# Kernel tuning notes

Hardware: AMD Instinct MI355X
Metric: run time of the kernel (lower is better)

## Reference

```python
import jax, jax.numpy as jnp
import numpy as np

MODES1 = 16
MODES2 = 16
KX_SIGMA = 1.0
B, T, H, W, C = 4, 32, 128, 128, 1

KY_KERNEL = np.array([[0.01, 0.02, 0.04, 0.02, 0.01],
                      [0.02, 0.06, 0.09, 0.06, 0.02],
                      [0.04, 0.09, 0.16, 0.09, 0.04],
                      [0.02, 0.06, 0.09, 0.06, 0.02],
                      [0.01, 0.02, 0.04, 0.02, 0.01]], dtype=np.float32)


def _spectral_mix(x, w1, w2):
    # x: (B,T,H,W,C); w1,w2: complex (C,C,m1,m2). FFT-mode-truncated mixing.
    b, t, h, w, c = x.shape
    xc = jnp.transpose(x, (0, 1, 4, 2, 3))            # (B,T,C,H,W)
    x_ft = jnp.fft.rfft2(xc)                          # (B,T,C,H,W//2+1)
    wr = w // 2 + 1
    out_ft = jnp.zeros((b, t, c, h, wr), dtype=x_ft.dtype)
    top = jnp.einsum('btixy,ioxy->btoxy', x_ft[:, :, :, :MODES1, :MODES2], w1)
    bot = jnp.einsum('btixy,ioxy->btoxy', x_ft[:, :, :, h - MODES1:, :MODES2], w2)
    out_ft = out_ft.at[:, :, :, :MODES1, :MODES2].set(top)
    out_ft = out_ft.at[:, :, :, h - MODES1:, :MODES2].set(bot)
    out = jnp.fft.irfft2(out_ft, s=(h, w))            # (B,T,C,H,W)
    return jnp.transpose(out, (0, 1, 3, 4, 2))


def _restricted_spectral(x, scalar):
    # diagonal (identity * scalar) spectral weights == scale truncated modes
    b, t, h, w, c = x.shape
    xc = jnp.transpose(x, (0, 1, 4, 2, 3))
    x_ft = jnp.fft.rfft2(xc)
    wr = w // 2 + 1
    out_ft = jnp.zeros((b, t, c, h, wr), dtype=x_ft.dtype)
    out_ft = out_ft.at[:, :, :, :MODES1, :MODES2].set(x_ft[:, :, :, :MODES1, :MODES2] * scalar)
    out_ft = out_ft.at[:, :, :, h - MODES1:, :MODES2].set(x_ft[:, :, :, h - MODES1:, :MODES2] * scalar)
    out = jnp.fft.irfft2(out_ft, s=(h, w))
    return jnp.transpose(out, (0, 1, 3, 4, 2))


def _circular_conv(value, kernel):
    # value: (B,T,H,W,1), kernel: (kh,kw); circular-pad cross-correlation
    b, t, h, w, _ = value.shape
    kh, kw = kernel.shape
    x = value.reshape(b * t, 1, h, w)
    xp = jnp.pad(x, ((0, 0), (0, 0), (kh // 2, kh - kh // 2 - 1), (kw // 2, kw - kw // 2 - 1)), mode='wrap')
    out = jax.lax.conv_general_dilated(xp, kernel[None, None], (1, 1), 'VALID',
                                       dimension_numbers=('NCHW', 'OIHW', 'NCHW'))
    return out.reshape(b, t, h, w, 1)


def setup_inputs() -> dict:
    key = jax.random.key(0)
    ks = jax.random.split(key, 10)
    z = jax.random.normal(ks[0], (B, T, 2 * H, W, C), dtype=jnp.float32)
    scale = 1.0 / (C * C)  # torch: scale * torch.rand(cfloat) -> uniform real & imag
    u = lambda k: scale * jax.random.uniform(k, (C, C, MODES1, MODES2), dtype=jnp.float32)
    return {
        'z': z,
        'qw1r': u(ks[1]), 'qw1i': u(ks[2]), 'qw2r': u(ks[3]), 'qw2i': u(ks[4]),
        'kw1r': u(ks[5]), 'kw1i': u(ks[6]), 'kw2r': u(ks[7]), 'kw2i': u(ks[8]),
        'icl_scalar': jnp.float32(0.1),
        'ky_kernel': jnp.asarray(KY_KERNEL),
    }


def reference(z, qw1r, qw1i, qw2r, qw2i, kw1r, kw1i, kw2r, kw2i, icl_scalar, ky_kernel):
    b, t, full_h, w, c = z.shape
    h = full_h // 2
    x, y = z[:, :, :h], z[:, :, h:]
    query = _spectral_mix(x, qw1r + 1j * qw1i, qw2r + 1j * qw2i)
    keyt = _spectral_mix(x, kw1r + 1j * kw1i, kw2r + 1j * kw2i)
    value = _restricted_spectral(y, icl_scalar)
    # laplacian kernel attention scores
    q_ = query.reshape(b, t, -1)
    k_ = keyt.reshape(b, t, -1)
    diff = q_[:, :, None, :] - k_[:, None, :, :]        # (B,T,T,H*W*C)
    l2 = jnp.sqrt(jnp.sum(diff * diff, axis=-1) + 1e-8)
    kx = jnp.exp(-l2 / KX_SIGMA)                         # (B,T,T)
    # mask: M @ kx zeros out last query row
    mask = jnp.concatenate([jnp.ones((t - 1,), jnp.float32), jnp.zeros((1,), jnp.float32)])
    kx = kx * mask[None, :, None]
    vc = _circular_conv(value, ky_kernel)                # (B,T,H,W,1)
    attn_y = jnp.einsum('bthwc,btq->bqhwc', vc, kx)      # (B,T,H,W,1)
    output = jnp.concatenate([jnp.zeros_like(x), attn_y], axis=2)
    return output, kx
```

## Files before the change

### kernel.cpp

```cpp
#include <hip/hip_runtime.h>
#include <math.h>

#define FVC_OFF   0
#define PHIQ_OFF  131072
#define PHIK_OFF  262144
#define OUT_KX_OFF 4194304

#define TWOPI_128 0.049087385212340517f

__global__ __launch_bounds__(256) void dft_rows_kernel(
    const float* __restrict__ z, float* __restrict__ Gout)
{
    __shared__ float ct[128], st[128];
    __shared__ float rows[16 * 132];
    __shared__ float2 tile[16 * 17];

    const int tid = threadIdx.x;
    const int img = blockIdx.x >> 3;
    const int c0  = blockIdx.x & 7;
    const int bt  = img & 127;
    const int isY = img >> 7;

    if (tid < 128) {
        float s, c;
        sincosf((float)tid * TWOPI_128, &s, &c);
        ct[tid] = c; st[tid] = s;
    }
    const float* xim = z + (size_t)bt * 32768 + (size_t)isY * 16384 + (size_t)c0 * 2048;
    {
        int q0 = tid, q1 = tid + 256;
        float4 a = *(const float4*)(xim + (q0 >> 5) * 128 + (q0 & 31) * 4);
        float4 b = *(const float4*)(xim + (q1 >> 5) * 128 + (q1 & 31) * 4);
        *(float4*)(rows + (q0 >> 5) * 132 + (q0 & 31) * 4) = a;
        *(float4*)(rows + (q1 >> 5) * 132 + (q1 & 31) * 4) = b;
    }
    __syncthreads();

    const int v  = tid & 15;
    const int hl = tid >> 4;
    float sr0 = 0.f, si0 = 0.f, sr1 = 0.f, si1 = 0.f;
    float sr2 = 0.f, si2 = 0.f, sr3 = 0.f, si3 = 0.f;
    const float4* rp = (const float4*)(rows + hl * 132);
    #pragma unroll 8
    for (int m = 0; m < 32; ++m) {
        float4 x4 = rp[m];
        int k = (v * m * 4) & 127;
        float c = ct[k], s = st[k];
        sr0 = fmaf(x4.x, c, sr0); si0 = fmaf(x4.x, s, si0);
        sr1 = fmaf(x4.y, c, sr1); si1 = fmaf(x4.y, s, si1);
        sr2 = fmaf(x4.z, c, sr2); si2 = fmaf(x4.z, s, si2);
        sr3 = fmaf(x4.w, c, sr3); si3 = fmaf(x4.w, s, si3);
    }
    float c1 = ct[v], s1 = st[v];
    float c2 = ct[(2 * v) & 127], s2 = st[(2 * v) & 127];
    float c3 = ct[(3 * v) & 127], s3 = st[(3 * v) & 127];
    float gr = sr0 + sr1 * c1 - si1 * s1 + sr2 * c2 - si2 * s2 + sr3 * c3 - si3 * s3;
    float gi = -(si0 + sr1 * s1 + si1 * c1 + sr2 * s2 + si2 * c2 + sr3 * s3 + si3 * c3);

    tile[v * 17 + hl] = make_float2(gr, gi);
    __syncthreads();
    const int vw = tid >> 4, hw = tid & 15;
    float2 val = tile[vw * 17 + hw];
    *(float2*)(Gout + (size_t)img * 4096 + vw * 256 + (c0 * 16 + hw) * 2) = val;
}

__global__ __launch_bounds__(128) void modes_kernel(
    const float* __restrict__ Gglob,
    const float* __restrict__ qw1r, const float* __restrict__ qw1i,
    const float* __restrict__ qw2r, const float* __restrict__ qw2i,
    const float* __restrict__ kw1r, const float* __restrict__ kw1i,
    const float* __restrict__ kw2r, const float* __restrict__ kw2i,
    const float* __restrict__ icl,  const float* __restrict__ ker,
    float* __restrict__ ws)
{
    __shared__ float ct[128], st[128];
    __shared__ float Gbuf[4 * 260];
    __shared__ float f0r[64], f0i[64];

    const int tid = threadIdx.x;
    const int img = blockIdx.x >> 2;
    const int vg  = blockIdx.x & 3;
    const int bt  = img & 127;
    const int isY = img >> 7;

    {
        float s, c;
        sincosf((float)tid * TWOPI_128, &s, &c);
        ct[tid] = c; st[tid] = s;
    }
    const float4* gsrc = (const float4*)(Gglob + (size_t)img * 4096 + (size_t)vg * 1024);
    {
        float4 a = gsrc[tid];
        float4 b = gsrc[tid + 128];
        *(float4*)(Gbuf + (tid >> 6) * 260 + (tid & 63) * 4) = a;
        *(float4*)(Gbuf + ((tid >> 6) + 2) * 260 + (tid & 63) * 4) = b;
    }
    __syncthreads();

    const int uu = tid & 31;
    const int vl = tid >> 5;
    const int v  = vg * 4 + vl;
    const int u  = (uu < 16) ? uu : uu + 96;

    float sr[4] = {0.f, 0.f, 0.f, 0.f}, si[4] = {0.f, 0.f, 0.f, 0.f};
    const float4* gp = (const float4*)(Gbuf + vl * 260);
    #pragma unroll 8
    for (int m = 0; m < 32; ++m) {
        float4 ga = gp[2 * m];
        float4 gb = gp[2 * m + 1];
        int k0 = (u * 4 * m) & 127;
        float c0 = ct[k0], s0 = st[k0];
        sr[0] = fmaf(ga.x, c0, fmaf(ga.y,  s0, sr[0]));
        si[0] = fmaf(ga.y, c0, fmaf(-ga.x, s0, si[0]));
        sr[1] = fmaf(ga.z, c0, fmaf(ga.w,  s0, sr[1]));
        si[1] = fmaf(ga.w, c0, fmaf(-ga.z, s0, si[1]));
        sr[2] = fmaf(gb.x, c0, fmaf(gb.y,  s0, sr[2]));
        si[2] = fmaf(gb.y, c0, fmaf(-gb.x, s0, si[2]));
        sr[3] = fmaf(gb.z, c0, fmaf(gb.w,  s0, sr[3]));
        si[3] = fmaf(gb.w, c0, fmaf(-gb.z, s0, si[3]));
    }
    float mr = sr[0], mi_ = si[0];
    #pragma unroll
    for (int j = 1; j < 4; ++j) {
        int k = (u * j) & 127;
        float cb = ct[k], sb = st[k];
        mr  += sr[j] * cb + si[j] * sb;
        mi_ += si[j] * cb - sr[j] * sb;
    }

    const int wi = (uu & 15) * 16 + v;

    if (!isY) {
        float a, bi_;
        if (uu < 16) { a = qw1r[wi]; bi_ = qw1i[wi]; }
        else         { a = qw2r[wi]; bi_ = qw2i[wi]; }
        float fqr = mr * a - mi_ * bi_;
        float fqi = mr * bi_ + mi_ * a;
        if (uu < 16) { a = kw1r[wi]; bi_ = kw1i[wi]; }
        else         { a = kw2r[wi]; bi_ = kw2i[wi]; }
        float fkr = mr * a - mi_ * bi_;
        float fki = mr * bi_ + mi_ * a;

        float* PQ = ws + PHIQ_OFF + (size_t)bt * 1024;
        float* PK = ws + PHIK_OFF + (size_t)bt * 1024;
        const float c2 = 0.011048543456039806f;
        if (v >= 1) {
            int o = ((v - 1) * 32 + uu) * 2;
            PQ[o] = c2 * fqr; PQ[o + 1] = c2 * fqi;
            PK[o] = c2 * fkr; PK[o + 1] = c2 * fki;
        } else {
            f0r[uu]      = fqr; f0i[uu]      = fqi;
            f0r[32 + uu] = fkr; f0i[32 + uu] = fki;
        }
        __syncthreads();
        if (vg == 0) {
            const float c1n = 0.0078125f;
            if (tid == 0) {
                PQ[960] = c1n * f0r[0];
                PK[960] = c1n * f0r[32];
            } else if (tid <= 15) {
                int uf = tid;
                float hr = 0.5f * (f0r[uf] + f0r[32 - uf]);
                float hi = 0.5f * (f0i[uf] - f0i[32 - uf]);
                int o = 961 + (uf - 1) * 2;
                PQ[o] = c2 * hr; PQ[o + 1] = c2 * hi;
                hr = 0.5f * (f0r[32 + uf] + f0r[32 + (32 - uf)]);
                hi = 0.5f * (f0i[32 + uf] - f0i[32 + (32 - uf)]);
                PK[o] = c2 * hr; PK[o + 1] = c2 * hi;
            } else if (tid == 16) {
                PQ[991] = c2 * 0.5f * f0r[16]; PQ[992] = -c2 * 0.5f * f0i[16];
                PK[991] = c2 * 0.5f * f0r[48]; PK[992] = -c2 * 0.5f * f0i[48];
            } else if (tid < 48) {
                PQ[993 + (tid - 17)] = 0.f;
                PK[993 + (tid - 17)] = 0.f;
            }
        }
    } else {
        float s = icl[0];
        float khr = 0.f, khi = 0.f;
        #pragma unroll
        for (int a2 = 0; a2 < 5; ++a2) {
            #pragma unroll
            for (int c3 = 0; c3 < 5; ++c3) {
                float kv = ker[a2 * 5 + c3];
                int e = (u * (a2 - 2) + v * (c3 - 2)) & 127;
                khr = fmaf(kv, ct[e], khr);
                khi = fmaf(kv, st[e], khi);
            }
        }
        const int slot = uu * 16 + v;
        float* FV = ws + FVC_OFF + (size_t)bt * 1024;
        FV[slot * 2]     = s * (mr * khr - mi_ * khi);
        FV[slot * 2 + 1] = s * (mr * khi + mi_ * khr);
    }
}

__global__ __launch_bounds__(256) void dist_mix_inv_kernel(
    const float* __restrict__ ws, float* __restrict__ out)
{
    __shared__ float ct[128], st[128];
    __shared__ float kxs[32];
    __shared__ float fmP[32 * 36];
    __shared__ float Ar[32 * 17], Ai[32 * 17];

    const int tid     = threadIdx.x;
    const int b       = blockIdx.x >> 7;
    const int rest    = blockIdx.x & 127;
    const int q       = rest >> 2;
    const int quarter = rest & 3;

    if (tid < 128) {
        float s, c;
        sincosf((float)tid * TWOPI_128, &s, &c);
        ct[tid] = c; st[tid] = s;
    }

    {
        const int t = tid >> 3, seg = tid & 7;
        const float4* qp = (const float4*)(ws + PHIQ_OFF + (size_t)(b * 32 + t) * 1024) + seg * 32;
        const float4* kp = (const float4*)(ws + PHIK_OFF + (size_t)(b * 32 + q) * 1024) + seg * 32;
        float acc = 0.f;
        #pragma unroll 8
        for (int d = 0; d < 32; ++d) {
            float4 qv = qp[d], kv = kp[d];
            float d0 = qv.x - kv.x, d1 = qv.y - kv.y;
            float d2 = qv.z - kv.z, d3 = qv.w - kv.w;
            acc = fmaf(d0, d0, acc); acc = fmaf(d1, d1, acc);
            acc = fmaf(d2, d2, acc); acc = fmaf(d3, d3, acc);
        }
        acc += __shfl_xor(acc, 1);
        acc += __shfl_xor(acc, 2);
        acc += __shfl_xor(acc, 4);
        if (seg == 0) {
            float l2  = sqrtf(acc + 1e-8f);
            float kxv = (t == 31) ? 0.f : expf(-l2);
            kxs[t] = kxv;
            if (quarter == 0)
                out[OUT_KX_OFF + (b * 32 + t) * 32 + q] = kxv;
        }
    }
    __syncthreads();

    {
        float4 acc = make_float4(0.f, 0.f, 0.f, 0.f);
        const float4* FV = (const float4*)(ws + FVC_OFF) + (size_t)b * 32 * 256;
        for (int i = 0; i < 31; ++i) {
            float kv = kxs[i];
            float4 f = FV[(size_t)i * 256 + tid];
            acc.x = fmaf(kv, f.x, acc.x);
            acc.y = fmaf(kv, f.y, acc.y);
            acc.z = fmaf(kv, f.z, acc.z);
            acc.w = fmaf(kv, f.w, acc.w);
        }
        int s0 = tid * 2;
        *(float4*)(fmP + (s0 >> 4) * 36 + (s0 & 15) * 2) = acc;
    }
    __syncthreads();

    {
        const int hl = tid >> 3;
        const int v0 = (tid & 7) * 2;
        const int h  = quarter * 32 + hl;
        float ar0 = 0.f, ai0 = 0.f, ar1 = 0.f, ai1 = 0.f;
        #pragma unroll 4
        for (int ui2 = 0; ui2 < 32; ++ui2) {
            int u = (ui2 < 16) ? ui2 : ui2 + 96;
            int k = (u * h) & 127;
            float cc = ct[k], ss = st[k];
            float4 f = *(const float4*)(fmP + ui2 * 36 + v0 * 2);
            ar0 = fmaf(f.x, cc, fmaf(-f.y, ss, ar0));
            ai0 = fmaf(f.x, ss, fmaf( f.y, cc, ai0));
            ar1 = fmaf(f.z, cc, fmaf(-f.w, ss, ar1));
            ai1 = fmaf(f.z, ss, fmaf( f.w, cc, ai1));
        }
        Ar[hl * 17 + v0]     = ar0; Ai[hl * 17 + v0]     = ai0;
        Ar[hl * 17 + v0 + 1] = ar1; Ai[hl * 17 + v0 + 1] = ai1;
    }
    __syncthreads();

    const int w2   = tid & 127;
    const int hpar = tid >> 7;
    float cw[16], sw[16];
    #pragma unroll
    for (int v = 1; v < 16; ++v) {
        int k = (v * w2) & 127;
        cw[v] = ct[k]; sw[v] = st[k];
    }
    const size_t obase = (size_t)(b * 32 + q) * 32768;
    for (int it = 0; it < 16; ++it) {
        int l = it * 2 + hpar;
        int r = quarter * 32 + l;
        const float* arp = Ar + l * 17;
        const float* aip = Ai + l * 17;
        float accp = arp[0];
        #pragma unroll
        for (int v = 1; v < 16; ++v)
            accp += 2.f * (arp[v] * cw[v] - aip[v] * sw[v]);
        out[obase + (size_t)r * 128 + w2] = 0.f;
        out[obase + (size_t)(128 + r) * 128 + w2] = accp * 6.103515625e-05f;
    }
}

extern "C" void kernel_launch(void* const* d_in, const int* in_sizes, int n_in,
                              void* d_out, int out_size, void* d_ws, size_t ws_size,
                              hipStream_t stream)
{
    (void)in_sizes; (void)n_in; (void)out_size; (void)ws_size;
    const float* z    = (const float*)d_in[0];
    const float* qw1r = (const float*)d_in[1];
    const float* qw1i = (const float*)d_in[2];
    const float* qw2r = (const float*)d_in[3];
    const float* qw2i = (const float*)d_in[4];
    const float* kw1r = (const float*)d_in[5];
    const float* kw1i = (const float*)d_in[6];
    const float* kw2r = (const float*)d_in[7];
    const float* kw2i = (const float*)d_in[8];
    const float* icl  = (const float*)d_in[9];
    const float* ker  = (const float*)d_in[10];
    float* ws  = (float*)d_ws;
    float* out = (float*)d_out;

    hipLaunchKernelGGL(dft_rows_kernel, dim3(2048), dim3(256), 0, stream, z, out);
    hipLaunchKernelGGL(modes_kernel, dim3(1024), dim3(128), 0, stream,
                       out, qw1r, qw1i, qw2r, qw2i, kw1r, kw1i, kw2r, kw2i,
                       icl, ker, ws);
    hipLaunchKernelGGL(dist_mix_inv_kernel, dim3(512), dim3(256), 0, stream, ws, out);
}
```

Baseline: 123.7 us.

## Use twiddle recurrences, float2 tables, half-period symmetry and early vector zero stores

The DFT loops now rotate their twiddle factors by complex multiplication instead of gathering cos/sin from indexed shared-memory tables, and the tables are packed as float2. The inverse W-direction pass uses the w and w+64 symmetry, computing even and odd harmonics once to produce two outputs per thread. The zero half of the output is written up front with float4 stores instead of scalar stores inside the final loop, and the Ar/Ai arrays are merged into one interleaved buffer. The aim is to cut LDS gathers, bank conflicts and arithmetic per output. The cost is a possible loss of float accuracy as rotation errors build up over 32 recurrence steps.

```diff
diff --git a/kernel.cpp b/kernel.cpp
--- a/kernel.cpp
+++ b/kernel.cpp
@@ -7,11 +7,12 @@
 #define OUT_KX_OFF 4194304
 
 #define TWOPI_128 0.049087385212340517f
+#define OUT_SCALE 6.103515625e-05f
 
 __global__ __launch_bounds__(256) void dft_rows_kernel(
     const float* __restrict__ z, float* __restrict__ Gout)
 {
-    __shared__ float ct[128], st[128];
+    __shared__ float2 tw[128];
     __shared__ float rows[16 * 132];
     __shared__ float2 tile[16 * 17];
 
@@ -24,7 +25,7 @@
     if (tid < 128) {
         float s, c;
         sincosf((float)tid * TWOPI_128, &s, &c);
-        ct[tid] = c; st[tid] = s;
+        tw[tid] = make_float2(c, s);
     }
     const float* xim = z + (size_t)bt * 32768 + (size_t)isY * 16384 + (size_t)c0 * 2048;
     {
@@ -38,24 +39,27 @@
 
     const int v  = tid & 15;
     const int hl = tid >> 4;
+    const float2 stp = tw[(4 * v) & 127];
+    float cc = 1.f, ss = 0.f;
     float sr0 = 0.f, si0 = 0.f, sr1 = 0.f, si1 = 0.f;
     float sr2 = 0.f, si2 = 0.f, sr3 = 0.f, si3 = 0.f;
     const float4* rp = (const float4*)(rows + hl * 132);
     #pragma unroll 8
     for (int m = 0; m < 32; ++m) {
         float4 x4 = rp[m];
-        int k = (v * m * 4) & 127;
-        float c = ct[k], s = st[k];
-        sr0 = fmaf(x4.x, c, sr0); si0 = fmaf(x4.x, s, si0);
-        sr1 = fmaf(x4.y, c, sr1); si1 = fmaf(x4.y, s, si1);
-        sr2 = fmaf(x4.z, c, sr2); si2 = fmaf(x4.z, s, si2);
-        sr3 = fmaf(x4.w, c, sr3); si3 = fmaf(x4.w, s, si3);
-    }
-    float c1 = ct[v], s1 = st[v];
-    float c2 = ct[(2 * v) & 127], s2 = st[(2 * v) & 127];
-    float c3 = ct[(3 * v) & 127], s3 = st[(3 * v) & 127];
-    float gr = sr0 + sr1 * c1 - si1 * s1 + sr2 * c2 - si2 * s2 + sr3 * c3 - si3 * s3;
-    float gi = -(si0 + sr1 * s1 + si1 * c1 + sr2 * s2 + si2 * c2 + sr3 * s3 + si3 * c3);
+        sr0 = fmaf(x4.x, cc, sr0); si0 = fmaf(x4.x, ss, si0);
+        sr1 = fmaf(x4.y, cc, sr1); si1 = fmaf(x4.y, ss, si1);
+        sr2 = fmaf(x4.z, cc, sr2); si2 = fmaf(x4.z, ss, si2);
+        sr3 = fmaf(x4.w, cc, sr3); si3 = fmaf(x4.w, ss, si3);
+        float t0 = fmaf(cc, stp.x, -(ss * stp.y));
+        float t1 = fmaf(cc, stp.y,  (ss * stp.x));
+        cc = t0; ss = t1;
+    }
+    float2 w1 = tw[v];
+    float2 w2 = tw[(2 * v) & 127];
+    float2 w3 = tw[(3 * v) & 127];
+    float gr = sr0 + sr1 * w1.x - si1 * w1.y + sr2 * w2.x - si2 * w2.y + sr3 * w3.x - si3 * w3.y;
+    float gi = -(si0 + sr1 * w1.y + si1 * w1.x + sr2 * w2.y + si2 * w2.x + sr3 * w3.y + si3 * w3.x);
 
     tile[v * 17 + hl] = make_float2(gr, gi);
     __syncthreads();
@@ -73,7 +77,7 @@
     const float* __restrict__ icl,  const float* __restrict__ ker,
     float* __restrict__ ws)
 {
-    __shared__ float ct[128], st[128];
+    __shared__ float2 tw[128];
     __shared__ float Gbuf[4 * 260];
     __shared__ float f0r[64], f0i[64];
 
@@ -86,7 +90,7 @@
     {
         float s, c;
         sincosf((float)tid * TWOPI_128, &s, &c);
-        ct[tid] = c; st[tid] = s;
+        tw[tid] = make_float2(c, s);
     }
     const float4* gsrc = (const float4*)(Gglob + (size_t)img * 4096 + (size_t)vg * 1024);
     {
@@ -102,30 +106,32 @@
     const int v  = vg * 4 + vl;
     const int u  = (uu < 16) ? uu : uu + 96;
 
+    const float2 stp = tw[(4 * u) & 127];
+    float cc = 1.f, ss = 0.f;
     float sr[4] = {0.f, 0.f, 0.f, 0.f}, si[4] = {0.f, 0.f, 0.f, 0.f};
     const float4* gp = (const float4*)(Gbuf + vl * 260);
     #pragma unroll 8
     for (int m = 0; m < 32; ++m) {
         float4 ga = gp[2 * m];
         float4 gb = gp[2 * m + 1];
-        int k0 = (u * 4 * m) & 127;
-        float c0 = ct[k0], s0 = st[k0];
-        sr[0] = fmaf(ga.x, c0, fmaf(ga.y,  s0, sr[0]));
-        si[0] = fmaf(ga.y, c0, fmaf(-ga.x, s0, si[0]));
-        sr[1] = fmaf(ga.z, c0, fmaf(ga.w,  s0, sr[1]));
-        si[1] = fmaf(ga.w, c0, fmaf(-ga.z, s0, si[1]));
-        sr[2] = fmaf(gb.x, c0, fmaf(gb.y,  s0, sr[2]));
-        si[2] = fmaf(gb.y, c0, fmaf(-gb.x, s0, si[2]));
-        sr[3] = fmaf(gb.z, c0, fmaf(gb.w,  s0, sr[3]));
-        si[3] = fmaf(gb.w, c0, fmaf(-gb.z, s0, si[3]));
+        sr[0] = fmaf(ga.x, cc, fmaf(ga.y,  ss, sr[0]));
+        si[0] = fmaf(ga.y, cc, fmaf(-ga.x, ss, si[0]));
+        sr[1] = fmaf(ga.z, cc, fmaf(ga.w,  ss, sr[1]));
+        si[1] = fmaf(ga.w, cc, fmaf(-ga.z, ss, si[1]));
+        sr[2] = fmaf(gb.x, cc, fmaf(gb.y,  ss, sr[2]));
+        si[2] = fmaf(gb.y, cc, fmaf(-gb.x, ss, si[2]));
+        sr[3] = fmaf(gb.z, cc, fmaf(gb.w,  ss, sr[3]));
+        si[3] = fmaf(gb.w, cc, fmaf(-gb.z, ss, si[3]));
+        float t0 = fmaf(cc, stp.x, -(ss * stp.y));
+        float t1 = fmaf(cc, stp.y,  (ss * stp.x));
+        cc = t0; ss = t1;
     }
     float mr = sr[0], mi_ = si[0];
     #pragma unroll
     for (int j = 1; j < 4; ++j) {
-        int k = (u * j) & 127;
-        float cb = ct[k], sb = st[k];
-        mr  += sr[j] * cb + si[j] * sb;
-        mi_ += si[j] * cb - sr[j] * sb;
+        float2 wj = tw[(u * j) & 127];
+        mr  += sr[j] * wj.x + si[j] * wj.y;
+        mi_ += si[j] * wj.x - sr[j] * wj.y;
     }
 
     const int wi = (uu & 15) * 16 + v;
@@ -183,9 +189,9 @@
             #pragma unroll
             for (int c3 = 0; c3 < 5; ++c3) {
                 float kv = ker[a2 * 5 + c3];
-                int e = (u * (a2 - 2) + v * (c3 - 2)) & 127;
-                khr = fmaf(kv, ct[e], khr);
-                khi = fmaf(kv, st[e], khi);
+                float2 e = tw[(u * (a2 - 2) + v * (c3 - 2)) & 127];
+                khr = fmaf(kv, e.x, khr);
+                khi = fmaf(kv, e.y, khi);
             }
         }
         const int slot = uu * 16 + v;
@@ -198,21 +204,31 @@
 __global__ __launch_bounds__(256) void dist_mix_inv_kernel(
     const float* __restrict__ ws, float* __restrict__ out)
 {
-    __shared__ float ct[128], st[128];
+    __shared__ float2 tw[128];
     __shared__ float kxs[32];
     __shared__ float fmP[32 * 36];
-    __shared__ float Ar[32 * 17], Ai[32 * 17];
+    __shared__ float Az[32 * 36];
 
     const int tid     = threadIdx.x;
     const int b       = blockIdx.x >> 7;
     const int rest    = blockIdx.x & 127;
     const int q       = rest >> 2;
     const int quarter = rest & 3;
+    const size_t obase = (size_t)(b * 32 + q) * 32768;
 
     if (tid < 128) {
         float s, c;
         sincosf((float)tid * TWOPI_128, &s, &c);
-        ct[tid] = c; st[tid] = s;
+        tw[tid] = make_float2(c, s);
+    }
+
+    {
+        const float4 z4 = make_float4(0.f, 0.f, 0.f, 0.f);
+        #pragma unroll
+        for (int k = 0; k < 4; ++k) {
+            int idx = k * 256 + tid;
+            *(float4*)(out + obase + (size_t)quarter * 4096 + (size_t)idx * 4) = z4;
+        }
     }
 
     {
@@ -261,43 +277,61 @@
         const int hl = tid >> 3;
         const int v0 = (tid & 7) * 2;
         const int h  = quarter * 32 + hl;
+        const float2 stp = tw[h];
+        float cA = 1.f, sA = 0.f;
+        const float2 ib = tw[(112 * h) & 127];
+        float cB = ib.x, sB = ib.y;
         float ar0 = 0.f, ai0 = 0.f, ar1 = 0.f, ai1 = 0.f;
         #pragma unroll 4
-        for (int ui2 = 0; ui2 < 32; ++ui2) {
-            int u = (ui2 < 16) ? ui2 : ui2 + 96;
-            int k = (u * h) & 127;
-            float cc = ct[k], ss = st[k];
-            float4 f = *(const float4*)(fmP + ui2 * 36 + v0 * 2);
-            ar0 = fmaf(f.x, cc, fmaf(-f.y, ss, ar0));
-            ai0 = fmaf(f.x, ss, fmaf( f.y, cc, ai0));
-            ar1 = fmaf(f.z, cc, fmaf(-f.w, ss, ar1));
-            ai1 = fmaf(f.z, ss, fmaf( f.w, cc, ai1));
-        }
-        Ar[hl * 17 + v0]     = ar0; Ai[hl * 17 + v0]     = ai0;
-        Ar[hl * 17 + v0 + 1] = ar1; Ai[hl * 17 + v0 + 1] = ai1;
-    }
-    __syncthreads();
-
-    const int w2   = tid & 127;
-    const int hpar = tid >> 7;
+        for (int j = 0; j < 16; ++j) {
+            float4 fa = *(const float4*)(fmP + j * 36 + v0 * 2);
+            ar0 = fmaf(fa.x, cA, fmaf(-fa.y, sA, ar0));
+            ai0 = fmaf(fa.x, sA, fmaf( fa.y, cA, ai0));
+            ar1 = fmaf(fa.z, cA, fmaf(-fa.w, sA, ar1));
+            ai1 = fmaf(fa.z, sA, fmaf( fa.w, cA, ai1));
+            float4 fb = *(const float4*)(fmP + (j + 16) * 36 + v0 * 2);
+            ar0 = fmaf(fb.x, cB, fmaf(-fb.y, sB, ar0));
+            ai0 = fmaf(fb.x, sB, fmaf( fb.y, cB, ai0));
+            ar1 = fmaf(fb.z, cB, fmaf(-fb.w, sB, ar1));
+            ai1 = fmaf(fb.z, sB, fmaf( fb.w, cB, ai1));
+            float t0 = fmaf(cA, stp.x, -(sA * stp.y));
+            float t1 = fmaf(cA, stp.y,  (sA * stp.x));
+            cA = t0; sA = t1;
+            t0 = fmaf(cB, stp.x, -(sB * stp.y));
+            t1 = fmaf(cB, stp.y,  (sB * stp.x));
+            cB = t0; sB = t1;
+        }
+        *(float4*)(Az + hl * 36 + v0 * 2) = make_float4(ar0, ai0, ar1, ai1);
+    }
+
+    const int wv   = tid >> 6;
+    const int lane = tid & 63;
     float cw[16], sw[16];
     #pragma unroll
     for (int v = 1; v < 16; ++v) {
-        int k = (v * w2) & 127;
-        cw[v] = ct[k]; sw[v] = st[k];
-    }
-    const size_t obase = (size_t)(b * 32 + q) * 32768;
-    for (int it = 0; it < 16; ++it) {
-        int l = it * 2 + hpar;
+        float2 t = tw[(v * lane) & 127];
+        cw[v] = t.x; sw[v] = t.y;
+    }
+    __syncthreads();
+
+    for (int lr = 0; lr < 8; ++lr) {
+        int l = wv * 8 + lr;
+        const float4* az = (const float4*)(Az + l * 36);
+        float4 f0 = az[0];
+        float base = f0.x;
+        float accO = f0.z * cw[1] - f0.w * sw[1];
+        float accE = 0.f;
+        #pragma unroll
+        for (int t2 = 1; t2 < 8; ++t2) {
+            float4 f = az[t2];
+            accE = fmaf(f.x, cw[2 * t2],     fmaf(-f.y, sw[2 * t2],     accE));
+            accO = fmaf(f.z, cw[2 * t2 + 1], fmaf(-f.w, sw[2 * t2 + 1], accO));
+        }
+        float pA = base + 2.f * (accE + accO);
+        float pB = base + 2.f * (accE - accO);
         int r = quarter * 32 + l;
-        const float* arp = Ar + l * 17;
-        const float* aip = Ai + l * 17;
-        float accp = arp[0];
-        #pragma unroll
-        for (int v = 1; v < 16; ++v)
-            accp += 2.f * (arp[v] * cw[v] - aip[v] * sw[v]);
-        out[obase + (size_t)r * 128 + w2] = 0.f;
-        out[obase + (size_t)(128 + r) * 128 + w2] = accp * 6.103515625e-05f;
+        out[obase + (size_t)(128 + r) * 128 + lane]      = pA * OUT_SCALE;
+        out[obase + (size_t)(128 + r) * 128 + lane + 64] = pB * OUT_SCALE;
     }
 }
 
```

New measurement: 116.3 us. -5.9%, faster.
